# Kernel tuning notes

Hardware: AMD Instinct MI355X
Metric: run time of the kernel (lower is better)

Reference implementation:

```python
import jax, jax.numpy as jnp
import numpy as np

D_MODEL = 1024
N_HEAD = 16
D_HEAD = D_MODEL // N_HEAD


def setup_inputs() -> dict:
    key = jax.random.key(0)
    ks = jax.random.split(key, 5)
    x = jax.random.normal(ks[0], (4, 2048, D_MODEL), dtype=jnp.float32)
    # qkv linear: weight [3*d_model, d_model], bias [3*d_model] (torch convention)
    w_qkv = jax.random.normal(ks[1], (3 * D_MODEL, D_MODEL), dtype=jnp.float32) / np.sqrt(D_MODEL)
    b_qkv = jnp.zeros((3 * D_MODEL,), dtype=jnp.float32)
    w_proj = jax.random.normal(ks[2], (D_MODEL, D_MODEL), dtype=jnp.float32) / np.sqrt(D_MODEL)
    b_proj = jnp.zeros((D_MODEL,), dtype=jnp.float32)
    return {"x": x, "w_qkv": w_qkv, "b_qkv": b_qkv, "w_proj": w_proj, "b_proj": b_proj}


def reference(x, w_qkv, b_qkv, w_proj, b_proj):
    B, T, C = x.shape
    qkv = x @ w_qkv.T + b_qkv  # [B,T,3C]
    q, k, v = jnp.split(qkv, 3, axis=-1)
    # [B, H, T, Dh]
    q = q.reshape(B, T, N_HEAD, D_HEAD).transpose(0, 2, 1, 3)
    k = k.reshape(B, T, N_HEAD, D_HEAD).transpose(0, 2, 1, 3)
    v = v.reshape(B, T, N_HEAD, D_HEAD).transpose(0, 2, 1, 3)
    att = jnp.einsum('bhqd,bhkd->bhqk', q, k) / jnp.sqrt(jnp.float32(D_HEAD))
    causal = jnp.tril(jnp.ones((T, T), dtype=bool))  # [T,T]
    att = jnp.where(causal, att, -jnp.inf)
    att = jax.nn.softmax(att, axis=-1)
    y = jnp.einsum('bhqk,bhkd->bhqd', att, v)  # [B,H,T,Dh]
    y = y.transpose(0, 2, 1, 3).reshape(B, T, C)
    return y @ w_proj.T + b_proj
```

## Files before the change

kernel.cpp:

```cpp
#include <hip/hip_runtime.h>
#include <hip/hip_bf16.h>

#define DEV static __device__ __forceinline__

typedef __attribute__((ext_vector_type(8))) short short8;
typedef __attribute__((ext_vector_type(4))) short short4v;
typedef __attribute__((ext_vector_type(4))) float float4v;
typedef __attribute__((ext_vector_type(4))) int int4v;

DEV unsigned short f2bf(float f) {
  unsigned int u = __builtin_bit_cast(unsigned int, f);
  u = (u + 0x7fffu + ((u >> 16) & 1u)) >> 16;
  return (unsigned short)u;
}

DEV __attribute__((address_space(3))) void* to_lds(void* p) {
  return (__attribute__((address_space(3))) void*)p;
}
DEV const __attribute__((address_space(1))) void* to_glb(const void* p) {
  return (const __attribute__((address_space(1))) void*)p;
}

DEV float4v zero4() { float4v z = {0.f, 0.f, 0.f, 0.f}; return z; }

DEV float ex2(float x) {
  float r;
  asm("v_exp_f32 %0, %1" : "=v"(r) : "v"(x));
  return r;
}
DEV unsigned int cvtpk(float lo, float hi) {
  unsigned int r;
  asm("v_cvt_pk_bf16_f32 %0, %1, %2" : "=v"(r) : "v"(lo), "v"(hi));
  return r;
}

__global__ __launch_bounds__(256)
void cvt3_kn(const float* __restrict__ x, const float* __restrict__ wq,
             const float* __restrict__ wp, unsigned short* __restrict__ xb,
             unsigned short* __restrict__ wqb, unsigned short* __restrict__ wpb) {
  const int NX = 8192 * 1024, NQ = 3072 * 1024, NP = 1024 * 1024;
  const int total = (NX + NQ + NP) / 4;
  int u = blockIdx.x * blockDim.x + threadIdx.x;
  int stride = gridDim.x * blockDim.x;
  for (; u < total; u += stride) {
    int i = u * 4;
    const float* s;
    unsigned short* d;
    if (i < NX) {
      s = x + i; d = xb + i;
    } else if (i < NX + NQ) {
      s = wq + (i - NX); d = wqb + (i - NX);
    } else {
      s = wp + (i - NX - NQ); d = wpb + (i - NX - NQ);
    }
    float4v v = *reinterpret_cast<const float4v*>(s);
    short4v o;
    o[0] = (short)f2bf(v[0]);
    o[1] = (short)f2bf(v[1]);
    o[2] = (short)f2bf(v[2]);
    o[3] = (short)f2bf(v[3]);
    *reinterpret_cast<short4v*>(d) = o;
  }
}

template<int EPI>
DEV void gemm_bt_body(const unsigned short* __restrict__ A, const unsigned short* __restrict__ B,
                      const float* __restrict__ bias, void* __restrict__ Cout,
                      unsigned short* __restrict__ vtout, int M, int N, int K,
                      unsigned short* sA, unsigned short* sB) {
  const int t = threadIdx.x;
  const int wave = t >> 6, lane = t & 63;
  const int wm = wave >> 1, wn = wave & 1;
  const int nwg = gridDim.x * gridDim.y;
  const int lid = blockIdx.y * gridDim.x + blockIdx.x;
  const int swz = (lid & 7) * (nwg >> 3) + (lid >> 3);
  const int m0 = (swz / gridDim.x) * 128, n0 = (swz % gridDim.x) * 128;
  const int l15 = lane & 15, l4 = lane >> 4;

  float4v acc[4][4];
#pragma unroll
  for (int i = 0; i < 4; i++)
#pragma unroll
    for (int j = 0; j < 4; j++) acc[i][j] = zero4();

  const int row_s = t >> 3;
  const int cols_s = ((t & 7) ^ ((t >> 3) & 7)) * 8;

  for (int k0 = 0; k0 < K; k0 += 64) {
    __syncthreads();
#pragma unroll
    for (int i = 0; i < 4; i++) {
      const unsigned short* ga = &A[(size_t)(m0 + row_s + i * 32) * K + k0 + cols_s];
      __builtin_amdgcn_global_load_lds(to_glb(ga), to_lds(&sA[(i * 4096 + wave * 1024) / 2]), 16, 0, 0);
    }
#pragma unroll
    for (int i = 0; i < 4; i++) {
      const unsigned short* gb = &B[(size_t)(n0 + row_s + i * 32) * K + k0 + cols_s];
      __builtin_amdgcn_global_load_lds(to_glb(gb), to_lds(&sB[(i * 4096 + wave * 1024) / 2]), 16, 0, 0);
    }
    __syncthreads();
#pragma unroll
    for (int kc = 0; kc < 2; kc++) {
      short8 af[4], bf[4];
#pragma unroll
      for (int mf = 0; mf < 4; mf++) {
        int off = ((wm * 64 + mf * 16 + l15) * 128 + kc * 64 + l4 * 16) ^ ((l15 & 7) << 4);
        af[mf] = *reinterpret_cast<const short8*>((const char*)sA + off);
      }
#pragma unroll
      for (int nf = 0; nf < 4; nf++) {
        int off = ((wn * 64 + nf * 16 + l15) * 128 + kc * 64 + l4 * 16) ^ ((l15 & 7) << 4);
        bf[nf] = *reinterpret_cast<const short8*>((const char*)sB + off);
      }
      __builtin_amdgcn_s_setprio(1);
#pragma unroll
      for (int mf = 0; mf < 4; mf++)
#pragma unroll
        for (int nf = 0; nf < 4; nf++)
          acc[mf][nf] = __builtin_amdgcn_mfma_f32_16x16x32_bf16(af[mf], bf[nf], acc[mf][nf], 0, 0, 0);
      __builtin_amdgcn_s_setprio(0);
    }
  }

#pragma unroll
  for (int mf = 0; mf < 4; mf++) {
    const int row0 = m0 + wm * 64 + mf * 16 + l4 * 4;
#pragma unroll
    for (int nf = 0; nf < 4; nf++) {
      const int col = n0 + wn * 64 + nf * 16 + l15;
      float vv[4];
#pragma unroll
      for (int r = 0; r < 4; r++) vv[r] = acc[mf][nf][r] + bias[col];
      if (EPI == 1) {
#pragma unroll
        for (int r = 0; r < 4; r++)
          ((float*)Cout)[(size_t)(row0 + r) * N + col] = vv[r];
      } else {
        if (col < 2048) {
          const float s = (col < 1024) ? 0.18033688f : 1.0f;
#pragma unroll
          for (int r = 0; r < 4; r++)
            ((unsigned short*)Cout)[(size_t)(row0 + r) * 2048 + col] = f2bf(vv[r] * s);
        } else {
          const int hv = col - 2048;
          const int R = ((row0 >> 11) * 16 + (hv >> 6)) * 64 + (hv & 63);
          const int tc = row0 & 2047;
          unsigned long long w = (unsigned long long)cvtpk(vv[0], vv[1]) |
                                 ((unsigned long long)cvtpk(vv[2], vv[3]) << 32);
          *(unsigned long long*)&vtout[(size_t)R * 2048 + tc] = w;
        }
      }
    }
  }
}

__global__ __launch_bounds__(256, 2)
void gemm_qkv_kn(const unsigned short* __restrict__ A, const unsigned short* __restrict__ B,
                 const float* __restrict__ bias, unsigned short* __restrict__ qkout,
                 unsigned short* __restrict__ vtout, int M, int N, int K) {
  __shared__ unsigned short sA[128 * 64];
  __shared__ unsigned short sB[128 * 64];
  gemm_bt_body<2>(A, B, bias, qkout, vtout, M, N, K, sA, sB);
}

__global__ __launch_bounds__(256, 2)
void gemm_proj_kn(const unsigned short* __restrict__ A, const unsigned short* __restrict__ B,
                  const float* __restrict__ bias, float* __restrict__ Cout,
                  int M, int N, int K) {
  __shared__ unsigned short sA[128 * 64];
  __shared__ unsigned short sB[128 * 64];
  gemm_bt_body<1>(A, B, bias, Cout, nullptr, M, N, K, sA, sB);
}

__global__ __launch_bounds__(256, 3)
void attn_kn(const unsigned short* __restrict__ qk, const unsigned short* __restrict__ vt,
             unsigned short* __restrict__ y) {
  __shared__ unsigned short sK[2][4096];
  __shared__ unsigned short sV[2][4096];
  __shared__ unsigned short sP[4][2048];
  const int t = threadIdx.x;
  const int wave = t >> 6, lane = t & 63;
  const int l15 = lane & 15, l4 = lane >> 4;
  const int bh = blockIdx.x, b = bh >> 4, h = bh & 15;
  const int yb_ = blockIdx.y;
  const int qt = ((yb_ >> 2) & 1) ? ((yb_ < 8) ? yb_ + 4 : yb_ - 12) : 15 - yb_;
  const int q0w = qt * 128 + wave * 32;
  const size_t base = (size_t)b * 2048 * 2048;
  const unsigned short* Qp = qk + base + h * 64;
  const unsigned short* Kp = Qp + 1024;
  const unsigned short* Vt = vt + (size_t)bh * 64 * 2048;
  unsigned short* yb = y + (size_t)b * 2048 * 1024 + h * 64;

  short8 ones8;
#pragma unroll
  for (int j = 0; j < 8; j++) ones8[j] = (short)0x3F80;

  short8 qf[2][2];
#pragma unroll
  for (int m = 0; m < 2; m++)
#pragma unroll
    for (int kc = 0; kc < 2; kc++)
      qf[m][kc] = *reinterpret_cast<const short8*>(
          &Qp[(size_t)(q0w + m * 16 + l15) * 2048 + kc * 32 + l4 * 8]);

  float4v o_acc[2][4];
#pragma unroll
  for (int m = 0; m < 2; m++)
#pragma unroll
    for (int f = 0; f < 4; f++) o_acc[m][f] = zero4();
  float4v acc_l[2] = {zero4(), zero4()};

  auto stage_k = [&](int kv0, int bi) {
#pragma unroll
    for (int i = 0; i < 2; i++) {
      int unit = t + i * 256;
      int row = unit >> 3, sl = unit & 7;
      const unsigned short* g = Kp + (size_t)(kv0 + row) * 2048 + (sl ^ (row & 7)) * 8;
      __builtin_amdgcn_global_load_lds(to_glb(g), to_lds(&sK[bi][unit * 8]), 16, 0, 0);
    }
  };
  auto stage_v = [&](int kv0, int bi) {
#pragma unroll
    for (int i = 0; i < 2; i++) {
      int unit = t + i * 256;
      int d = unit >> 3, sl = unit & 7;
      const unsigned short* g = Vt + (size_t)d * 2048 + kv0 + (sl ^ (d & 7)) * 8;
      __builtin_amdgcn_global_load_lds(to_glb(g), to_lds(&sV[bi][unit * 8]), 16, 0, 0);
    }
  };

  const int nt = 2 * qt + 2;
  stage_k(0, 0);
  stage_v(0, 0);
  __syncthreads();

  for (int ti = 0; ti < nt; ti++) {
    const int cur = ti & 1;
    const int kv0 = ti * 64;
    const bool last = (ti + 1 == nt);
    if (!last) { stage_k(kv0 + 64, cur ^ 1); stage_v(kv0 + 64, cur ^ 1); }

    if (kv0 <= q0w + 31) {
      const char* Kb = (const char*)sK[cur];
      const char* Vb = (const char*)sV[cur];
      char* Pb = (char*)sP[wave];

      float4v st[2][4];
#pragma unroll
      for (int m = 0; m < 2; m++)
#pragma unroll
        for (int c = 0; c < 4; c++) st[m][c] = zero4();
#pragma unroll
      for (int kc = 0; kc < 2; kc++) {
        short8 ka[4];
#pragma unroll
        for (int c = 0; c < 4; c++) {
          int off = ((c * 16 + l15) * 128 + kc * 64 + l4 * 16) ^ ((l15 & 7) << 4);
          ka[c] = *reinterpret_cast<const short8*>(Kb + off);
        }
        __builtin_amdgcn_s_setprio(1);
#pragma unroll
        for (int c = 0; c < 4; c++) {
          st[0][c] = __builtin_amdgcn_mfma_f32_16x16x32_bf16(ka[c], qf[0][kc], st[0][c], 0, 0, 0);
          st[1][c] = __builtin_amdgcn_mfma_f32_16x16x32_bf16(ka[c], qf[1][kc], st[1][c], 0, 0, 0);
        }
        __builtin_amdgcn_s_setprio(0);
      }

#pragma unroll
      for (int m = 0; m < 2; m++) {
        if (kv0 + 63 > q0w + m * 16) {
          const int qrow = q0w + m * 16 + l15;
#pragma unroll
          for (int c = 0; c < 4; c++)
#pragma unroll
            for (int r = 0; r < 4; r++) {
              int kv = kv0 + c * 16 + l4 * 4 + r;
              if (kv > qrow) st[m][c][r] = -1e30f;
            }
        }
#pragma unroll
        for (int c = 0; c < 4; c++) {
          float p0 = ex2(st[m][c][0]), p1 = ex2(st[m][c][1]);
          float p2 = ex2(st[m][c][2]), p3 = ex2(st[m][c][3]);
          unsigned long long w = (unsigned long long)cvtpk(p0, p1) |
                                 ((unsigned long long)cvtpk(p2, p3) << 32);
          int off = ((m * 16 + l15) * 128 + (c * 16 + l4 * 4) * 2) ^ ((l15 & 7) << 4);
          *(unsigned long long*)(Pb + off) = w;
        }
      }
      asm volatile("s_waitcnt lgkmcnt(0)" ::: "memory");
      __builtin_amdgcn_sched_barrier(0);

#pragma unroll
      for (int kc = 0; kc < 2; kc++) {
        short8 pa[2];
#pragma unroll
        for (int m = 0; m < 2; m++) {
          int off = ((m * 16 + l15) * 128 + kc * 64 + l4 * 16) ^ ((l15 & 7) << 4);
          pa[m] = *reinterpret_cast<const short8*>(Pb + off);
        }
        short8 vbf[4];
#pragma unroll
        for (int f = 0; f < 4; f++) {
          int d = f * 16 + l15;
          int off = (d * 128 + kc * 64 + l4 * 16) ^ ((d & 7) << 4);
          vbf[f] = *reinterpret_cast<const short8*>(Vb + off);
        }
        __builtin_amdgcn_s_setprio(1);
#pragma unroll
        for (int f = 0; f < 4; f++) {
          o_acc[0][f] = __builtin_amdgcn_mfma_f32_16x16x32_bf16(pa[0], vbf[f], o_acc[0][f], 0, 0, 0);
          o_acc[1][f] = __builtin_amdgcn_mfma_f32_16x16x32_bf16(pa[1], vbf[f], o_acc[1][f], 0, 0, 0);
        }
        acc_l[0] = __builtin_amdgcn_mfma_f32_16x16x32_bf16(pa[0], ones8, acc_l[0], 0, 0, 0);
        acc_l[1] = __builtin_amdgcn_mfma_f32_16x16x32_bf16(pa[1], ones8, acc_l[1], 0, 0, 0);
        __builtin_amdgcn_s_setprio(0);
      }
    }
    __syncthreads();
  }

#pragma unroll
  for (int m = 0; m < 2; m++) {
    float lr[4];
#pragma unroll
    for (int r = 0; r < 4; r++) lr[r] = 1.0f / acc_l[m][r];
#pragma unroll
    for (int f = 0; f < 4; f++)
#pragma unroll
      for (int r = 0; r < 4; r++) {
        int q = q0w + m * 16 + l4 * 4 + r;
        yb[(size_t)q * 1024 + f * 16 + l15] = f2bf(o_acc[m][f][r] * lr[r]);
      }
  }
}

extern "C" void kernel_launch(void* const* d_in, const int* in_sizes, int n_in,
                              void* d_out, int out_size, void* d_ws, size_t ws_size,
                              hipStream_t stream) {
  const float* x = (const float*)d_in[0];
  const float* w_qkv = (const float*)d_in[1];
  const float* b_qkv = (const float*)d_in[2];
  const float* w_proj = (const float*)d_in[3];
  const float* b_proj = (const float*)d_in[4];
  float* out = (float*)d_out;
  char* ws = (char*)d_ws;

  const int M = 4 * 2048;
  unsigned short* x_bf = (unsigned short*)ws;
  unsigned short* wqkv_bf = (unsigned short*)(ws + (22ull << 20));
  unsigned short* wproj_bf = (unsigned short*)(ws + (28ull << 20));
  unsigned short* qk_buf = (unsigned short*)(ws + (30ull << 20));
  unsigned short* vt = (unsigned short*)(ws + (62ull << 20));
  unsigned short* y_bf = x_bf;

  cvt3_kn<<<2048, 256, 0, stream>>>(x, w_qkv, w_proj, x_bf, wqkv_bf, wproj_bf);

  gemm_qkv_kn<<<dim3(24, 64), 256, 0, stream>>>(
      x_bf, wqkv_bf, b_qkv, qk_buf, vt, M, 3072, 1024);

  attn_kn<<<dim3(64, 16), 256, 0, stream>>>(qk_buf, vt, y_bf);

  gemm_proj_kn<<<dim3(8, 64), 256, 0, stream>>>(
      y_bf, wproj_bf, b_proj, out, M, 1024, 1024);
}
```

Baseline: 152.5 us.

## Pair mirrored causal query tiles per attention block for load balance

Each attention block now processes two query row sets, a low one (L) and its mirrored high one (H = 2016 - L). Every block therefore does about the same amount of causal work, and each staged K/V tile is reused by both query sets. The grid is halved to 64x8, P buffers and accumulators double, and launch bounds drop from 3 to 2 waves-per-SIMD occupancy, which raises register pressure and lowers occupancy. The code also relies on the existing no-max softmax, which assumes bounded scores.

```diff
diff --git a/kernel.cpp b/kernel.cpp
--- a/kernel.cpp
+++ b/kernel.cpp
@@ -172,19 +172,19 @@
   gemm_bt_body<1>(A, B, bias, Cout, nullptr, M, N, K, sA, sB);
 }
 
-__global__ __launch_bounds__(256, 3)
+__global__ __launch_bounds__(256, 2)
 void attn_kn(const unsigned short* __restrict__ qk, const unsigned short* __restrict__ vt,
              unsigned short* __restrict__ y) {
   __shared__ unsigned short sK[2][4096];
   __shared__ unsigned short sV[2][4096];
-  __shared__ unsigned short sP[4][2048];
+  __shared__ unsigned short sP[4][2][2048];
   const int t = threadIdx.x;
   const int wave = t >> 6, lane = t & 63;
   const int l15 = lane & 15, l4 = lane >> 4;
   const int bh = blockIdx.x, b = bh >> 4, h = bh & 15;
   const int yb_ = blockIdx.y;
-  const int qt = ((yb_ >> 2) & 1) ? ((yb_ < 8) ? yb_ + 4 : yb_ - 12) : 15 - yb_;
-  const int q0w = qt * 128 + wave * 32;
+  const int L = yb_ * 128 + wave * 32;
+  const int H = 2016 - L;
   const size_t base = (size_t)b * 2048 * 2048;
   const unsigned short* Qp = qk + base + h * 64;
   const unsigned short* Kp = Qp + 1024;
@@ -195,20 +195,26 @@
 #pragma unroll
   for (int j = 0; j < 8; j++) ones8[j] = (short)0x3F80;
 
-  short8 qf[2][2];
-#pragma unroll
-  for (int m = 0; m < 2; m++)
-#pragma unroll
-    for (int kc = 0; kc < 2; kc++)
-      qf[m][kc] = *reinterpret_cast<const short8*>(
-          &Qp[(size_t)(q0w + m * 16 + l15) * 2048 + kc * 32 + l4 * 8]);
-
-  float4v o_acc[2][4];
-#pragma unroll
-  for (int m = 0; m < 2; m++)
-#pragma unroll
-    for (int f = 0; f < 4; f++) o_acc[m][f] = zero4();
-  float4v acc_l[2] = {zero4(), zero4()};
+  short8 qf[2][2][2];
+#pragma unroll
+  for (int s = 0; s < 2; s++) {
+    const int q0 = s ? H : L;
+#pragma unroll
+    for (int m = 0; m < 2; m++)
+#pragma unroll
+      for (int kc = 0; kc < 2; kc++)
+        qf[s][m][kc] = *reinterpret_cast<const short8*>(
+            &Qp[(size_t)(q0 + m * 16 + l15) * 2048 + kc * 32 + l4 * 8]);
+  }
+
+  float4v o_acc[2][2][4];
+#pragma unroll
+  for (int s = 0; s < 2; s++)
+#pragma unroll
+    for (int m = 0; m < 2; m++)
+#pragma unroll
+      for (int f = 0; f < 4; f++) o_acc[s][m][f] = zero4();
+  float4v acc_l[2][2] = {{zero4(), zero4()}, {zero4(), zero4()}};
 
   auto stage_k = [&](int kv0, int bi) {
 #pragma unroll
@@ -229,7 +235,7 @@
     }
   };
 
-  const int nt = 2 * qt + 2;
+  const int nt = 32 - 2 * yb_;
   stage_k(0, 0);
   stage_v(0, 0);
   __syncthreads();
@@ -240,16 +246,20 @@
     const bool last = (ti + 1 == nt);
     if (!last) { stage_k(kv0 + 64, cur ^ 1); stage_v(kv0 + 64, cur ^ 1); }
 
-    if (kv0 <= q0w + 31) {
+    const bool act0 = (kv0 <= L + 31);
+    const bool act1 = (kv0 <= H + 31);
+
+    if (act0 | act1) {
       const char* Kb = (const char*)sK[cur];
       const char* Vb = (const char*)sV[cur];
-      char* Pb = (char*)sP[wave];
-
-      float4v st[2][4];
-#pragma unroll
-      for (int m = 0; m < 2; m++)
-#pragma unroll
-        for (int c = 0; c < 4; c++) st[m][c] = zero4();
+
+      float4v st[2][2][4];
+#pragma unroll
+      for (int s = 0; s < 2; s++)
+#pragma unroll
+        for (int m = 0; m < 2; m++)
+#pragma unroll
+          for (int c = 0; c < 4; c++) st[s][m][c] = zero4();
 #pragma unroll
       for (int kc = 0; kc < 2; kc++) {
         short8 ka[4];
@@ -259,34 +269,49 @@
           ka[c] = *reinterpret_cast<const short8*>(Kb + off);
         }
         __builtin_amdgcn_s_setprio(1);
-#pragma unroll
-        for (int c = 0; c < 4; c++) {
-          st[0][c] = __builtin_amdgcn_mfma_f32_16x16x32_bf16(ka[c], qf[0][kc], st[0][c], 0, 0, 0);
-          st[1][c] = __builtin_amdgcn_mfma_f32_16x16x32_bf16(ka[c], qf[1][kc], st[1][c], 0, 0, 0);
+        if (act0) {
+#pragma unroll
+          for (int c = 0; c < 4; c++)
+#pragma unroll
+            for (int m = 0; m < 2; m++)
+              st[0][m][c] = __builtin_amdgcn_mfma_f32_16x16x32_bf16(ka[c], qf[0][m][kc], st[0][m][c], 0, 0, 0);
+        }
+        if (act1) {
+#pragma unroll
+          for (int c = 0; c < 4; c++)
+#pragma unroll
+            for (int m = 0; m < 2; m++)
+              st[1][m][c] = __builtin_amdgcn_mfma_f32_16x16x32_bf16(ka[c], qf[1][m][kc], st[1][m][c], 0, 0, 0);
         }
         __builtin_amdgcn_s_setprio(0);
       }
 
 #pragma unroll
-      for (int m = 0; m < 2; m++) {
-        if (kv0 + 63 > q0w + m * 16) {
-          const int qrow = q0w + m * 16 + l15;
-#pragma unroll
-          for (int c = 0; c < 4; c++)
-#pragma unroll
-            for (int r = 0; r < 4; r++) {
-              int kv = kv0 + c * 16 + l4 * 4 + r;
-              if (kv > qrow) st[m][c][r] = -1e30f;
-            }
-        }
-#pragma unroll
-        for (int c = 0; c < 4; c++) {
-          float p0 = ex2(st[m][c][0]), p1 = ex2(st[m][c][1]);
-          float p2 = ex2(st[m][c][2]), p3 = ex2(st[m][c][3]);
-          unsigned long long w = (unsigned long long)cvtpk(p0, p1) |
-                                 ((unsigned long long)cvtpk(p2, p3) << 32);
-          int off = ((m * 16 + l15) * 128 + (c * 16 + l4 * 4) * 2) ^ ((l15 & 7) << 4);
-          *(unsigned long long*)(Pb + off) = w;
+      for (int s = 0; s < 2; s++) {
+        if (!(s ? act1 : act0)) continue;
+        const int q0s = s ? H : L;
+        char* Pb = (char*)sP[wave][s];
+#pragma unroll
+        for (int m = 0; m < 2; m++) {
+          if (kv0 + 63 > q0s + m * 16) {
+            const int qrow = q0s + m * 16 + l15;
+#pragma unroll
+            for (int c = 0; c < 4; c++)
+#pragma unroll
+              for (int r = 0; r < 4; r++) {
+                int kv = kv0 + c * 16 + l4 * 4 + r;
+                if (kv > qrow) st[s][m][c][r] = -1e30f;
+              }
+          }
+#pragma unroll
+          for (int c = 0; c < 4; c++) {
+            float p0 = ex2(st[s][m][c][0]), p1 = ex2(st[s][m][c][1]);
+            float p2 = ex2(st[s][m][c][2]), p3 = ex2(st[s][m][c][3]);
+            unsigned long long w = (unsigned long long)cvtpk(p0, p1) |
+                                   ((unsigned long long)cvtpk(p2, p3) << 32);
+            int off = ((m * 16 + l15) * 128 + (c * 16 + l4 * 4) * 2) ^ ((l15 & 7) << 4);
+            *(unsigned long long*)(Pb + off) = w;
+          }
         }
       }
       asm volatile("s_waitcnt lgkmcnt(0)" ::: "memory");
@@ -294,12 +319,6 @@
 
 #pragma unroll
       for (int kc = 0; kc < 2; kc++) {
-        short8 pa[2];
-#pragma unroll
-        for (int m = 0; m < 2; m++) {
-          int off = ((m * 16 + l15) * 128 + kc * 64 + l4 * 16) ^ ((l15 & 7) << 4);
-          pa[m] = *reinterpret_cast<const short8*>(Pb + off);
-        }
         short8 vbf[4];
 #pragma unroll
         for (int f = 0; f < 4; f++) {
@@ -307,32 +326,48 @@
           int off = (d * 128 + kc * 64 + l4 * 16) ^ ((d & 7) << 4);
           vbf[f] = *reinterpret_cast<const short8*>(Vb + off);
         }
-        __builtin_amdgcn_s_setprio(1);
-#pragma unroll
-        for (int f = 0; f < 4; f++) {
-          o_acc[0][f] = __builtin_amdgcn_mfma_f32_16x16x32_bf16(pa[0], vbf[f], o_acc[0][f], 0, 0, 0);
-          o_acc[1][f] = __builtin_amdgcn_mfma_f32_16x16x32_bf16(pa[1], vbf[f], o_acc[1][f], 0, 0, 0);
-        }
-        acc_l[0] = __builtin_amdgcn_mfma_f32_16x16x32_bf16(pa[0], ones8, acc_l[0], 0, 0, 0);
-        acc_l[1] = __builtin_amdgcn_mfma_f32_16x16x32_bf16(pa[1], ones8, acc_l[1], 0, 0, 0);
-        __builtin_amdgcn_s_setprio(0);
+#pragma unroll
+        for (int s = 0; s < 2; s++) {
+          if (!(s ? act1 : act0)) continue;
+          const char* Pb = (const char*)sP[wave][s];
+          short8 pa[2];
+#pragma unroll
+          for (int m = 0; m < 2; m++) {
+            int off = ((m * 16 + l15) * 128 + kc * 64 + l4 * 16) ^ ((l15 & 7) << 4);
+            pa[m] = *reinterpret_cast<const short8*>(Pb + off);
+          }
+          __builtin_amdgcn_s_setprio(1);
+#pragma unroll
+          for (int f = 0; f < 4; f++)
+#pragma unroll
+            for (int m = 0; m < 2; m++)
+              o_acc[s][m][f] = __builtin_amdgcn_mfma_f32_16x16x32_bf16(pa[m], vbf[f], o_acc[s][m][f], 0, 0, 0);
+#pragma unroll
+          for (int m = 0; m < 2; m++)
+            acc_l[s][m] = __builtin_amdgcn_mfma_f32_16x16x32_bf16(pa[m], ones8, acc_l[s][m], 0, 0, 0);
+          __builtin_amdgcn_s_setprio(0);
+        }
       }
     }
     __syncthreads();
   }
 
 #pragma unroll
-  for (int m = 0; m < 2; m++) {
-    float lr[4];
-#pragma unroll
-    for (int r = 0; r < 4; r++) lr[r] = 1.0f / acc_l[m][r];
-#pragma unroll
-    for (int f = 0; f < 4; f++)
-#pragma unroll
-      for (int r = 0; r < 4; r++) {
-        int q = q0w + m * 16 + l4 * 4 + r;
-        yb[(size_t)q * 1024 + f * 16 + l15] = f2bf(o_acc[m][f][r] * lr[r]);
-      }
+  for (int s = 0; s < 2; s++) {
+    const int q0s = s ? H : L;
+#pragma unroll
+    for (int m = 0; m < 2; m++) {
+      float lr[4];
+#pragma unroll
+      for (int r = 0; r < 4; r++) lr[r] = 1.0f / acc_l[s][m][r];
+#pragma unroll
+      for (int f = 0; f < 4; f++)
+#pragma unroll
+        for (int r = 0; r < 4; r++) {
+          int q = q0s + m * 16 + l4 * 4 + r;
+          yb[(size_t)q * 1024 + f * 16 + l15] = f2bf(o_acc[s][m][f][r] * lr[r]);
+        }
+    }
   }
 }
 
@@ -360,7 +395,7 @@
   gemm_qkv_kn<<<dim3(24, 64), 256, 0, stream>>>(
       x_bf, wqkv_bf, b_qkv, qk_buf, vt, M, 3072, 1024);
 
-  attn_kn<<<dim3(64, 16), 256, 0, stream>>>(qk_buf, vt, y_bf);
+  attn_kn<<<dim3(64, 8), 256, 0, stream>>>(qk_buf, vt, y_bf);
 
   gemm_proj_kn<<<dim3(8, 64), 256, 0, stream>>>(
       y_bf, wproj_bf, b_proj, out, M, 1024, 1024);
```

New measurement: 158.6 us. +4.0%, slower.
